# Kernel tuning notes

Measured on AMD Instinct MI355X. Metric: run time of the kernel, lower is better.

The kernel has to match this reference:

```python
import jax, jax.numpy as jnp
import numpy as np

N_NODES = 50000
N_EDGES = 800000
IN_F, HID, OUT_F = 128, 128, 64


def setup_inputs() -> dict:
    key = jax.random.key(0)
    k1, k2, k3, k4 = jax.random.split(key, 4)
    x = jax.random.normal(k1, (N_NODES, IN_F), dtype=jnp.float32)
    edge_index = jax.random.randint(k2, (2, N_EDGES), 0, N_NODES, dtype=jnp.int64)
    # Glorot-style scaled weights, zero bias (PyG GCNConv default)
    W1 = jax.random.normal(k3, (IN_F, HID), dtype=jnp.float32) * (1.0 / np.sqrt(IN_F))
    b1 = jnp.zeros((HID,), dtype=jnp.float32)
    W2 = jax.random.normal(k4, (HID, OUT_F), dtype=jnp.float32) * (1.0 / np.sqrt(HID))
    b2 = jnp.zeros((OUT_F,), dtype=jnp.float32)
    return {"x": x, "edge_index": edge_index, "W1": W1, "b1": b1, "W2": W2, "b2": b2}


def reference(x, edge_index, W1, b1, W2, b2):
    n = x.shape[0]
    # add self-loops (PyG GCNConv default add_self_loops=True)
    loop = jnp.arange(n, dtype=edge_index.dtype)
    src = jnp.concatenate([edge_index[0], loop])  # message source nodes
    dst = jnp.concatenate([edge_index[1], loop])  # aggregation target nodes
    # symmetric normalization: D^{-1/2} (A+I) D^{-1/2}
    deg = jax.ops.segment_sum(jnp.ones(dst.shape, dtype=x.dtype), dst, num_segments=n)
    dinv = jnp.where(deg > 0, jax.lax.rsqrt(deg), 0.0)
    norm = dinv[src] * dinv[dst]  # [E+N]

    def gcn_conv(h, W, b):
        h = h @ W                              # dense transform first (PyG order)
        msg = h[src] * norm[:, None]           # gather + scale: [E+N, d]
        agg = jax.ops.segment_sum(msg, dst, num_segments=n)  # scatter-add
        return agg + b

    h = jax.nn.relu(gcn_conv(x, W1, b1))
    return gcn_conv(h, W2, b2)
```

## Files before the change

### kernel.cpp

```cpp
#include <hip/hip_runtime.h>
#include <hip/hip_bf16.h>

#define NN   50000
#define NE   800000
#define F_IN 128
#define F_H  128
#define F_O  64

#define BINSHIFT 7
#define NBINS    ((NN + 127) >> 7)
#define CAP      2816
#define EPB      2048
#define RPSTRIDE 132

static constexpr int NB_G1  = (NN + 63) / 64;
static constexpr int NB_BIN = (NE + EPB - 1) / EPB;

typedef __bf16 bf16_8 __attribute__((ext_vector_type(8)));
typedef float  f32x4  __attribute__((ext_vector_type(4)));

template <typename AT, int K, int NOUT>
__device__ __forceinline__ void gemm_body(const AT* __restrict__ X,
                                          const float* __restrict__ W,
                                          __hip_bfloat16* __restrict__ Y,
                                          __hip_bfloat16* WB, int blk) {
    constexpr int NKS = K / 32;
    constexpr int NC  = NOUT / 16;
    const int t = threadIdx.x;
    for (int f = t; f < K * NOUT; f += 256) {
        int k = f / NOUT, n = f % NOUT;
        int ks = k >> 5, kr = k & 31, qq = kr >> 3, jj = kr & 7;
        int c = n >> 4, nn = n & 15;
        WB[(((ks * NC + c) * 16 + nn) * 4 + qq) * 8 + jj] = __float2bfloat16(W[f]);
    }
    __syncthreads();

    const int wave = t >> 6, lane = t & 63;
    const int r = lane & 15, q = lane >> 4;
    const int m0 = blk * 64 + wave * 16;
    int arow = m0 + r;
    if (arow >= NN) arow = NN - 1;

    f32x4 acc[NC];
#pragma unroll
    for (int c = 0; c < NC; ++c) acc[c] = (f32x4){0.f, 0.f, 0.f, 0.f};

#pragma unroll
    for (int ks = 0; ks < NKS; ++ks) {
        bf16_8 a;
        if constexpr (sizeof(AT) == 4) {
            const float* xp = (const float*)X + (size_t)arow * K + ks * 32 + q * 8;
            float4 x0 = ((const float4*)xp)[0];
            float4 x1 = ((const float4*)xp)[1];
            a[0] = (__bf16)x0.x; a[1] = (__bf16)x0.y; a[2] = (__bf16)x0.z; a[3] = (__bf16)x0.w;
            a[4] = (__bf16)x1.x; a[5] = (__bf16)x1.y; a[6] = (__bf16)x1.z; a[7] = (__bf16)x1.w;
        } else {
            a = *(const bf16_8*)((const __hip_bfloat16*)X + (size_t)arow * K + ks * 32 + q * 8);
        }
#pragma unroll
        for (int c = 0; c < NC; ++c) {
            bf16_8 b = *(const bf16_8*)&WB[(((ks * NC + c) * 16 + r) * 4 + q) * 8];
            acc[c] = __builtin_amdgcn_mfma_f32_16x16x32_bf16(a, b, acc[c], 0, 0, 0);
        }
    }

#pragma unroll
    for (int c = 0; c < NC; ++c) {
#pragma unroll
        for (int i = 0; i < 4; ++i) {
            int gr = m0 + q * 4 + i;
            if (gr < NN)
                Y[(size_t)gr * NOUT + c * 16 + r] = __float2bfloat16(acc[c][i]);
        }
    }
}

__global__ __launch_bounds__(256) void k_fuseA(const float* __restrict__ X,
                                               const float* __restrict__ W1,
                                               __hip_bfloat16* __restrict__ Xw,
                                               const int* __restrict__ ei32,
                                               int* __restrict__ binbuf,
                                               unsigned* __restrict__ bincnt,
                                               unsigned* __restrict__ cnt) {
    __shared__ __align__(16) char smem[32768];
    const int t = threadIdx.x;

    if (blockIdx.x >= NB_BIN) {
        gemm_body<float, F_IN, F_H>(X, W1, Xw, (__hip_bfloat16*)smem,
                                    blockIdx.x - NB_BIN);
        return;
    }

    unsigned* hist = (unsigned*)smem;
    unsigned* base = hist + NBINS;
    unsigned* rank = base + NBINS;
    for (int i = t; i < NBINS; i += 256) { hist[i] = 0u; rank[i] = 0u; }
    __syncthreads();

    const bool is64 = ((ei32[1] | ei32[3] | ei32[5] | ei32[7]) == 0);
    const int e0 = blockIdx.x * EPB;
    int pk[8], bin[8], dd[8];
#pragma unroll
    for (int j = 0; j < 8; ++j) {
        int e = e0 + t + j * 256;
        if (e < NE) {
            int s, d;
            if (is64) {
                const long long* p = (const long long*)ei32;
                s = (int)p[e];
                d = (int)p[NE + e];
            } else {
                s = ei32[e];
                d = ei32[NE + e];
            }
            pk[j]  = (s << BINSHIFT) | (d & 127);
            bin[j] = d >> BINSHIFT;
            dd[j]  = d;
        } else bin[j] = -1;
    }
#pragma unroll
    for (int j = 0; j < 8; ++j) {
        if (bin[j] >= 0) {
            atomicAdd(&hist[bin[j]], 1u);
            atomicAdd(&cnt[dd[j]], 1u);
        }
    }
    __syncthreads();
    for (int b = t; b < NBINS; b += 256)
        base[b] = atomicAdd(&bincnt[b], hist[b]);
    __syncthreads();
#pragma unroll
    for (int j = 0; j < 8; ++j) {
        if (bin[j] >= 0) {
            unsigned rk = atomicAdd(&rank[bin[j]], 1u);
            binbuf[(size_t)bin[j] * CAP + base[bin[j]] + rk] = pk[j];
        }
    }
}

#define HS 136
__global__ __launch_bounds__(1024) void k_phaseC(const int* __restrict__ binbuf,
                                                 const unsigned* __restrict__ bincnt,
                                                 const unsigned* __restrict__ cnt,
                                                 const __hip_bfloat16* __restrict__ Xw,
                                                 const float* __restrict__ W2,
                                                 const float* __restrict__ b1,
                                                 __hip_bfloat16* __restrict__ Hw,
                                                 int* __restrict__ srcs_g,
                                                 unsigned short* __restrict__ rp_g) {
    __shared__ __align__(16) char smem[64000];
    __hip_bfloat16* Htile = (__hip_bfloat16*)smem;
    __hip_bfloat16* WB2   = (__hip_bfloat16*)(smem + 34816);
    int*      srcsL = (int*)(smem + 34816 + 16384);
    unsigned* h     = (unsigned*)(smem + 62464);
    unsigned* cur   = (unsigned*)(smem + 62976);
    float*    dv    = (float*)(smem + 63488);

    const int b = blockIdx.x, t = threadIdx.x;

    for (int f = t; f < F_H * F_O; f += 1024) {
        int k = f / F_O, n = f % F_O;
        int ks = k >> 5, kr = k & 31, qq = kr >> 3, jj = kr & 7;
        int c = n >> 4, nn = n & 15;
        WB2[(((ks * 4 + c) * 16 + nn) * 4 + qq) * 8 + jj] = __float2bfloat16(W2[f]);
    }
    if (t < 128) h[t] = 0u;
    __syncthreads();

    const unsigned n = bincnt[b];
    const int* buf = binbuf + (size_t)b * CAP;
    for (unsigned i = t; i < n; i += 1024)
        atomicAdd(&h[buf[i] & 127], 1u);
    __syncthreads();
    if (t < 128) cur[t] = h[t];
    __syncthreads();
    for (int off = 1; off < 128; off <<= 1) {
        unsigned u = (t < 128 && t >= off) ? cur[t - off] : 0u;
        __syncthreads();
        if (t < 128) cur[t] += u;
        __syncthreads();
    }
    if (t < 128) {
        unsigned ex = cur[t] - h[t];
        rp_g[b * RPSTRIDE + t] = (unsigned short)ex;
        if (t == 0) rp_g[b * RPSTRIDE + 128] = (unsigned short)n;
        dv[t]  = rsqrtf((float)(h[t] + 1u));
        cur[t] = ex;
    }
    __syncthreads();
    for (unsigned i = t; i < n; i += 1024) {
        int p = buf[i];
        unsigned pos = atomicAdd(&cur[p & 127], 1u);
        int s = p >> BINSHIFT;
        srcsL[pos] = s;
        srcs_g[(size_t)b * CAP + pos] = s;
    }
    __syncthreads();

    const int wave = t >> 6, lane = t & 63;
    const int fl = lane & 15, sub = lane >> 4;
    const float4 b1a = ((const float4*)b1)[fl * 2];
    const float4 b1b = ((const float4*)b1)[fl * 2 + 1];
    for (int nd = 0; nd < 8; ++nd) {
        const int tl    = wave * 8 + nd;
        const int gnode = (b << BINSHIFT) + tl;
        const unsigned i1 = cur[tl];
        const unsigned i0 = i1 - h[tl];
        float acc0[8], acc1[8];
        {
            int sv = (gnode < NN) ? gnode : 0;
            bf16_8 r = *(const bf16_8*)(Xw + (size_t)sv * F_H + fl * 8);
            float w = (sub == 0 && gnode < NN) ? dv[tl] : 0.f;
#pragma unroll
            for (int j = 0; j < 8; ++j) { acc0[j] = w * (float)r[j]; acc1[j] = 0.f; }
        }
        unsigned i = i0 + sub;
        for (; i + 4 < i1; i += 8) {
            int s0 = srcsL[i], s1 = srcsL[i + 4];
            float w0 = rsqrtf((float)(cnt[s0] + 1u));
            float w1 = rsqrtf((float)(cnt[s1] + 1u));
            bf16_8 r0 = *(const bf16_8*)(Xw + (size_t)s0 * F_H + fl * 8);
            bf16_8 r1 = *(const bf16_8*)(Xw + (size_t)s1 * F_H + fl * 8);
#pragma unroll
            for (int j = 0; j < 8; ++j) {
                acc0[j] += w0 * (float)r0[j];
                acc1[j] += w1 * (float)r1[j];
            }
        }
        if (i < i1) {
            int s = srcsL[i];
            float w = rsqrtf((float)(cnt[s] + 1u));
            bf16_8 r = *(const bf16_8*)(Xw + (size_t)s * F_H + fl * 8);
#pragma unroll
            for (int j = 0; j < 8; ++j) acc0[j] += w * (float)r[j];
        }
#pragma unroll
        for (int j = 0; j < 8; ++j) {
            float a = acc0[j] + acc1[j];
            a += __shfl_xor(a, 16, 64);
            a += __shfl_xor(a, 32, 64);
            acc0[j] = a;
        }
        if (sub == 0) {
            const float bias[8] = {b1a.x, b1a.y, b1a.z, b1a.w, b1b.x, b1b.y, b1b.z, b1b.w};
            bf16_8 o;
#pragma unroll
            for (int j = 0; j < 8; ++j)
                o[j] = (__bf16)fmaxf(dv[tl] * acc0[j] + bias[j], 0.f);
            *(bf16_8*)(Htile + tl * HS + fl * 8) = o;
        }
    }
    __syncthreads();

    {
        const int r = lane & 15, q = lane >> 4;
        const int rt = wave >> 1;
        const int c0 = (wave & 1) * 2;
        f32x4 acc[2] = {(f32x4){0.f, 0.f, 0.f, 0.f}, (f32x4){0.f, 0.f, 0.f, 0.f}};
#pragma unroll
        for (int ks = 0; ks < 4; ++ks) {
            bf16_8 a = *(const bf16_8*)(Htile + (rt * 16 + r) * HS + ks * 32 + q * 8);
#pragma unroll
            for (int cc = 0; cc < 2; ++cc) {
                bf16_8 bb = *(const bf16_8*)&WB2[(((ks * 4 + (c0 + cc)) * 16 + r) * 4 + q) * 8];
                acc[cc] = __builtin_amdgcn_mfma_f32_16x16x32_bf16(a, bb, acc[cc], 0, 0, 0);
            }
        }
#pragma unroll
        for (int cc = 0; cc < 2; ++cc) {
#pragma unroll
            for (int i = 0; i < 4; ++i) {
                int tl = rt * 16 + q * 4 + i;
                int gnode = (b << BINSHIFT) + tl;
                if (gnode < NN)
                    Hw[(size_t)gnode * F_O + (c0 + cc) * 16 + r] =
                        __float2bfloat16(dv[tl] * acc[cc][i]);
            }
        }
    }
}

__global__ __launch_bounds__(256) void k_agg2(const __hip_bfloat16* __restrict__ Hw,
                                              const int* __restrict__ srcs_g,
                                              const unsigned short* __restrict__ rp_g,
                                              const float* __restrict__ b2,
                                              float* __restrict__ out) {
    const int wv   = (blockIdx.x * 256 + threadIdx.x) >> 6;
    const int lane = threadIdx.x & 63;
    if (wv >= NN) return;
    const int bin = wv >> BINSHIFT, tl = wv & 127;
    const int sub = lane >> 3;
    const int fl  = lane & 7;
    const unsigned i0 = rp_g[bin * RPSTRIDE + tl];
    const unsigned i1 = rp_g[bin * RPSTRIDE + tl + 1];
    const int* srcs = srcs_g + (size_t)bin * CAP;

    float acc0[8], acc1[8];
    bf16_8 self = *(const bf16_8*)(Hw + (size_t)wv * F_O + fl * 8);
#pragma unroll
    for (int j = 0; j < 8; ++j) {
        acc0[j] = (sub == 0) ? (float)self[j] : 0.f;
        acc1[j] = 0.f;
    }

    unsigned i = i0 + sub;
    for (; i + 8 < i1; i += 16) {
        int s0 = srcs[i], s1 = srcs[i + 8];
        bf16_8 r0 = *(const bf16_8*)(Hw + (size_t)s0 * F_O + fl * 8);
        bf16_8 r1 = *(const bf16_8*)(Hw + (size_t)s1 * F_O + fl * 8);
#pragma unroll
        for (int j = 0; j < 8; ++j) {
            acc0[j] += (float)r0[j];
            acc1[j] += (float)r1[j];
        }
    }
    if (i < i1) {
        int s = srcs[i];
        bf16_8 r = *(const bf16_8*)(Hw + (size_t)s * F_O + fl * 8);
#pragma unroll
        for (int j = 0; j < 8; ++j) acc0[j] += (float)r[j];
    }
#pragma unroll
    for (int j = 0; j < 8; ++j) {
        float a = acc0[j] + acc1[j];
        a += __shfl_xor(a, 8, 64);
        a += __shfl_xor(a, 16, 64);
        a += __shfl_xor(a, 32, 64);
        acc0[j] = a;
    }
    if (sub == 0) {
        float dn = rsqrtf((float)(i1 - i0 + 1u));
        float4 o0 = make_float4(dn * acc0[0] + b2[fl * 8 + 0], dn * acc0[1] + b2[fl * 8 + 1],
                                dn * acc0[2] + b2[fl * 8 + 2], dn * acc0[3] + b2[fl * 8 + 3]);
        float4 o1 = make_float4(dn * acc0[4] + b2[fl * 8 + 4], dn * acc0[5] + b2[fl * 8 + 5],
                                dn * acc0[6] + b2[fl * 8 + 6], dn * acc0[7] + b2[fl * 8 + 7]);
        float4* op = (float4*)(out + (size_t)wv * F_O + fl * 8);
        op[0] = o0;
        op[1] = o1;
    }
}

extern "C" void kernel_launch(void* const* d_in, const int* in_sizes, int n_in,
                              void* d_out, int out_size, void* d_ws, size_t ws_size,
                              hipStream_t stream) {
    const float* x  = (const float*)d_in[0];
    const int*   ei = (const int*)d_in[1];
    const float* W1 = (const float*)d_in[2];
    const float* b1 = (const float*)d_in[3];
    const float* W2 = (const float*)d_in[4];
    const float* b2 = (const float*)d_in[5];
    float* out = (float*)d_out;

    char* w = (char*)d_ws;
    size_t off = 0;
    auto alloc = [&](size_t bytes) {
        void* p = w + off;
        off += (bytes + 255) & ~(size_t)255;
        return p;
    };
    unsigned* cnt     = (unsigned*)alloc((size_t)NN * 4);
    unsigned* bincnt  = (unsigned*)alloc((size_t)NBINS * 4);
    int*      binbuf  = (int*)alloc((size_t)NBINS * CAP * 4);
    int*      srcs    = (int*)alloc((size_t)NBINS * CAP * 4);
    unsigned short* rp = (unsigned short*)alloc((size_t)NBINS * RPSTRIDE * 2);
    __hip_bfloat16* Xw = (__hip_bfloat16*)alloc((size_t)NN * F_H * 2);
    __hip_bfloat16* Hw = (__hip_bfloat16*)alloc((size_t)NN * F_O * 2);

    size_t zlen = (((size_t)NN * 4 + 255) & ~(size_t)255) + (size_t)NBINS * 4;
    hipMemsetAsync(cnt, 0, zlen, stream);

    k_fuseA<<<NB_BIN + NB_G1, 256, 0, stream>>>(x, W1, Xw, ei, binbuf, bincnt, cnt);
    k_phaseC<<<NBINS, 1024, 0, stream>>>(binbuf, bincnt, cnt, Xw, W2, b1, Hw, srcs, rp);
    k_agg2<<<(NN + 3) / 4, 256, 0, stream>>>(Hw, srcs, rp, b2, out);
}
```

Baseline: 199.4 us.

## Fuse phase C and layer-2 aggregation into cooperative kernel with grid syncs

Replaces the global atomic bin counters and the memset with per-block local binning, where each block writes its own prefix-sum table and segment. The second and third kernels are merged into one cooperative kernel with 391 blocks of 512 threads. It gathers each bin's edges from all block segments, builds a CSR in LDS, publishes dinv globally, and uses grid.sync between layer 1, the W2 GEMM and layer 2, so the CSR stays in shared memory. This removes the memset, one launch and the global srcs/rp round trip. In exchange it adds a binary-search gather, two grid-wide barriers and a requirement that all 391 blocks are co-resident.

```diff
diff --git a/kernel.cpp b/kernel.cpp
--- a/kernel.cpp
+++ b/kernel.cpp
@@ -1,5 +1,8 @@
 #include <hip/hip_runtime.h>
 #include <hip/hip_bf16.h>
+#include <hip/hip_cooperative_groups.h>
+
+namespace cg = cooperative_groups;
 
 #define NN   50000
 #define NE   800000
@@ -10,34 +13,35 @@
 #define BINSHIFT 7
 #define NBINS    ((NN + 127) >> 7)
 #define CAP      2816
-#define EPB      2048
-#define RPSTRIDE 132
-
-static constexpr int NB_G1  = (NN + 63) / 64;
-static constexpr int NB_BIN = (NE + EPB - 1) / EPB;
+#define EPB      8192
+#define RSS      (NBINS + 1)
+#define HS       132
+
+static constexpr int NB_GEMM = (NN + 127) / 128;
+static constexpr int NB_BIN  = (NE + EPB - 1) / EPB;
 
 typedef __bf16 bf16_8 __attribute__((ext_vector_type(8)));
 typedef float  f32x4  __attribute__((ext_vector_type(4)));
 
 template <typename AT, int K, int NOUT>
-__device__ __forceinline__ void gemm_body(const AT* __restrict__ X,
-                                          const float* __restrict__ W,
-                                          __hip_bfloat16* __restrict__ Y,
-                                          __hip_bfloat16* WB, int blk) {
+__device__ __forceinline__ void gemm_body512(const AT* __restrict__ X,
+                                             const float* __restrict__ W,
+                                             __hip_bfloat16* __restrict__ Y,
+                                             __hip_bfloat16* WB, int blk) {
     constexpr int NKS = K / 32;
     constexpr int NC  = NOUT / 16;
     const int t = threadIdx.x;
-    for (int f = t; f < K * NOUT; f += 256) {
+    for (int f = t; f < K * NOUT; f += 512) {
         int k = f / NOUT, n = f % NOUT;
         int ks = k >> 5, kr = k & 31, qq = kr >> 3, jj = kr & 7;
         int c = n >> 4, nn = n & 15;
-        WB[(((ks * NC + c) * 16 + nn) * 4 + qq) * 8 + jj] = __float2bfloat16(W[f]);
+        WB[(((ks * NC + c) * 4 + qq) * 16 + nn) * 8 + jj] = __float2bfloat16(W[f]);
     }
     __syncthreads();
 
     const int wave = t >> 6, lane = t & 63;
     const int r = lane & 15, q = lane >> 4;
-    const int m0 = blk * 64 + wave * 16;
+    const int m0 = blk * 128 + wave * 16;
     int arow = m0 + r;
     if (arow >= NN) arow = NN - 1;
 
@@ -59,7 +63,7 @@
         }
 #pragma unroll
         for (int c = 0; c < NC; ++c) {
-            bf16_8 b = *(const bf16_8*)&WB[(((ks * NC + c) * 16 + r) * 4 + q) * 8];
+            bf16_8 b = *(const bf16_8*)&WB[(((ks * NC + c) * 4 + q) * 16 + r) * 8];
             acc[c] = __builtin_amdgcn_mfma_f32_16x16x32_bf16(a, b, acc[c], 0, 0, 0);
         }
     }
@@ -75,102 +79,122 @@
     }
 }
 
-__global__ __launch_bounds__(256) void k_fuseA(const float* __restrict__ X,
+__global__ __launch_bounds__(512) void k_fuseA(const float* __restrict__ X,
                                                const float* __restrict__ W1,
                                                __hip_bfloat16* __restrict__ Xw,
                                                const int* __restrict__ ei32,
                                                int* __restrict__ binbuf,
-                                               unsigned* __restrict__ bincnt,
-                                               unsigned* __restrict__ cnt) {
+                                               unsigned* __restrict__ rs) {
     __shared__ __align__(16) char smem[32768];
     const int t = threadIdx.x;
 
     if (blockIdx.x >= NB_BIN) {
-        gemm_body<float, F_IN, F_H>(X, W1, Xw, (__hip_bfloat16*)smem,
-                                    blockIdx.x - NB_BIN);
+        gemm_body512<float, F_IN, F_H>(X, W1, Xw, (__hip_bfloat16*)smem,
+                                       blockIdx.x - NB_BIN);
         return;
     }
 
     unsigned* hist = (unsigned*)smem;
-    unsigned* base = hist + NBINS;
-    unsigned* rank = base + NBINS;
-    for (int i = t; i < NBINS; i += 256) { hist[i] = 0u; rank[i] = 0u; }
+    unsigned* ofs  = hist + 512;
+    for (int i = t; i < NBINS; i += 512) hist[i] = 0u;
     __syncthreads();
 
     const bool is64 = ((ei32[1] | ei32[3] | ei32[5] | ei32[7]) == 0);
+    const long long* p64 = (const long long*)ei32;
     const int e0 = blockIdx.x * EPB;
-    int pk[8], bin[8], dd[8];
-#pragma unroll
-    for (int j = 0; j < 8; ++j) {
-        int e = e0 + t + j * 256;
-        if (e < NE) {
-            int s, d;
-            if (is64) {
-                const long long* p = (const long long*)ei32;
-                s = (int)p[e];
-                d = (int)p[NE + e];
-            } else {
-                s = ei32[e];
-                d = ei32[NE + e];
-            }
-            pk[j]  = (s << BINSHIFT) | (d & 127);
-            bin[j] = d >> BINSHIFT;
-            dd[j]  = d;
-        } else bin[j] = -1;
-    }
-#pragma unroll
-    for (int j = 0; j < 8; ++j) {
-        if (bin[j] >= 0) {
-            atomicAdd(&hist[bin[j]], 1u);
-            atomicAdd(&cnt[dd[j]], 1u);
-        }
-    }
-    __syncthreads();
-    for (int b = t; b < NBINS; b += 256)
-        base[b] = atomicAdd(&bincnt[b], hist[b]);
-    __syncthreads();
-#pragma unroll
-    for (int j = 0; j < 8; ++j) {
-        if (bin[j] >= 0) {
-            unsigned rk = atomicAdd(&rank[bin[j]], 1u);
-            binbuf[(size_t)bin[j] * CAP + base[bin[j]] + rk] = pk[j];
-        }
+    const int e1 = (e0 + EPB < NE) ? e0 + EPB : NE;
+
+    for (int e = e0 + t; e < e1; e += 512) {
+        int d = is64 ? (int)p64[NE + e] : ei32[NE + e];
+        atomicAdd(&hist[d >> BINSHIFT], 1u);
+    }
+    __syncthreads();
+
+    unsigned v = (t < NBINS) ? hist[t] : 0u;
+    ofs[t] = v;
+    __syncthreads();
+    for (int off = 1; off < 512; off <<= 1) {
+        unsigned u = (t >= off) ? ofs[t - off] : 0u;
+        __syncthreads();
+        ofs[t] += u;
+        __syncthreads();
+    }
+    if (t < NBINS) {
+        unsigned ex = ofs[t] - v;
+        rs[blockIdx.x * RSS + t] = ex;
+        hist[t] = ex;
+    }
+    if (t == 0) rs[blockIdx.x * RSS + NBINS] = (unsigned)(e1 - e0);
+    __syncthreads();
+
+    for (int e = e0 + t; e < e1; e += 512) {
+        int s, d;
+        if (is64) { s = (int)p64[e]; d = (int)p64[NE + e]; }
+        else      { s = ei32[e];     d = ei32[NE + e]; }
+        unsigned pos = atomicAdd(&hist[d >> BINSHIFT], 1u);
+        binbuf[e0 + pos] = (s << BINSHIFT) | (d & 127);
     }
 }
 
-#define HS 136
-__global__ __launch_bounds__(1024) void k_phaseC(const int* __restrict__ binbuf,
-                                                 const unsigned* __restrict__ bincnt,
-                                                 const unsigned* __restrict__ cnt,
-                                                 const __hip_bfloat16* __restrict__ Xw,
-                                                 const float* __restrict__ W2,
-                                                 const float* __restrict__ b1,
-                                                 __hip_bfloat16* __restrict__ Hw,
-                                                 int* __restrict__ srcs_g,
-                                                 unsigned short* __restrict__ rp_g) {
-    __shared__ __align__(16) char smem[64000];
+__global__ __launch_bounds__(512) void k_mega(const int* __restrict__ binbuf,
+                                              const unsigned* __restrict__ rs,
+                                              const __hip_bfloat16* __restrict__ Xw,
+                                              const float* __restrict__ W2,
+                                              const float* __restrict__ b1,
+                                              const float* __restrict__ b2,
+                                              float* __restrict__ dinvG,
+                                              __hip_bfloat16* __restrict__ Hw,
+                                              float* __restrict__ out) {
+    cg::grid_group grid = cg::this_grid();
+
+    __shared__ __align__(16) char smem[64512];
     __hip_bfloat16* Htile = (__hip_bfloat16*)smem;
-    __hip_bfloat16* WB2   = (__hip_bfloat16*)(smem + 34816);
-    int*      srcsL = (int*)(smem + 34816 + 16384);
-    unsigned* h     = (unsigned*)(smem + 62464);
-    unsigned* cur   = (unsigned*)(smem + 62976);
-    float*    dv    = (float*)(smem + 63488);
-
-    const int b = blockIdx.x, t = threadIdx.x;
-
-    for (int f = t; f < F_H * F_O; f += 1024) {
-        int k = f / F_O, n = f % F_O;
-        int ks = k >> 5, kr = k & 31, qq = kr >> 3, jj = kr & 7;
-        int c = n >> 4, nn = n & 15;
-        WB2[(((ks * 4 + c) * 16 + nn) * 4 + qq) * 8 + jj] = __float2bfloat16(W2[f]);
-    }
-    if (t < 128) h[t] = 0u;
-    __syncthreads();
-
-    const unsigned n = bincnt[b];
-    const int* buf = binbuf + (size_t)b * CAP;
-    for (unsigned i = t; i < n; i += 1024)
-        atomicAdd(&h[buf[i] & 127], 1u);
+    int*      srcsL = (int*)smem;
+    int*      csrL  = (int*)(smem + 33792);
+    __hip_bfloat16* W2B = (__hip_bfloat16*)(smem + 45056);
+    unsigned* stL  = (unsigned*)(smem + 61440);
+    unsigned* lenL = (unsigned*)(smem + 61952);
+    unsigned* lofs = (unsigned*)(smem + 62464);
+    unsigned* h    = (unsigned*)(smem + 62976);
+    unsigned* cur  = (unsigned*)(smem + 63488);
+    float*    dv   = (float*)(smem + 64000);
+
+    const int bb = blockIdx.x, t = threadIdx.x;
+    const int wave = t >> 6, lane = t & 63;
+
+    if (t < 128) {
+        unsigned s0 = 0, ln = 0;
+        if (t < NB_BIN) {
+            s0 = rs[t * RSS + bb];
+            ln = rs[t * RSS + bb + 1] - s0;
+        }
+        stL[t] = s0;
+        lenL[t] = ln;
+        lofs[t] = ln;
+        h[t] = 0u;
+    }
+    __syncthreads();
+    for (int off = 1; off < 128; off <<= 1) {
+        unsigned u = (t < 128 && t >= off) ? lofs[t - off] : 0u;
+        __syncthreads();
+        if (t < 128) lofs[t] += u;
+        __syncthreads();
+    }
+    const unsigned n = lofs[NB_BIN - 1];
+
+    for (unsigned i = t; i < n; i += 512) {
+        int lo = 0, hi = NB_BIN - 1;
+        while (lo < hi) {
+            int mid = (lo + hi) >> 1;
+            if (lofs[mid] > i) hi = mid; else lo = mid + 1;
+        }
+        unsigned within = i - (lofs[lo] - lenL[lo]);
+        srcsL[i] = binbuf[lo * EPB + stL[lo] + within];
+    }
+    __syncthreads();
+
+    for (unsigned i = t; i < n; i += 512)
+        atomicAdd(&h[srcsL[i] & 127], 1u);
     __syncthreads();
     if (t < 128) cur[t] = h[t];
     __syncthreads();
@@ -182,161 +206,177 @@
     }
     if (t < 128) {
         unsigned ex = cur[t] - h[t];
-        rp_g[b * RPSTRIDE + t] = (unsigned short)ex;
-        if (t == 0) rp_g[b * RPSTRIDE + 128] = (unsigned short)n;
-        dv[t]  = rsqrtf((float)(h[t] + 1u));
+        int node = (bb << BINSHIFT) + t;
+        float d = rsqrtf((float)(h[t] + 1u));
+        dv[t] = d;
+        if (node < NN) dinvG[node] = d;
         cur[t] = ex;
     }
     __syncthreads();
-    for (unsigned i = t; i < n; i += 1024) {
-        int p = buf[i];
+    for (unsigned i = t; i < n; i += 512) {
+        int p = srcsL[i];
         unsigned pos = atomicAdd(&cur[p & 127], 1u);
-        int s = p >> BINSHIFT;
-        srcsL[pos] = s;
-        srcs_g[(size_t)b * CAP + pos] = s;
-    }
-    __syncthreads();
-
-    const int wave = t >> 6, lane = t & 63;
-    const int fl = lane & 15, sub = lane >> 4;
-    const float4 b1a = ((const float4*)b1)[fl * 2];
-    const float4 b1b = ((const float4*)b1)[fl * 2 + 1];
-    for (int nd = 0; nd < 8; ++nd) {
-        const int tl    = wave * 8 + nd;
-        const int gnode = (b << BINSHIFT) + tl;
-        const unsigned i1 = cur[tl];
-        const unsigned i0 = i1 - h[tl];
-        float acc0[8], acc1[8];
+        csrL[pos] = p >> BINSHIFT;
+    }
+
+    grid.sync();
+
+    {
+        const int sub = lane >> 4, fl = lane & 15;
+        float b1r[8];
         {
-            int sv = (gnode < NN) ? gnode : 0;
-            bf16_8 r = *(const bf16_8*)(Xw + (size_t)sv * F_H + fl * 8);
-            float w = (sub == 0 && gnode < NN) ? dv[tl] : 0.f;
-#pragma unroll
-            for (int j = 0; j < 8; ++j) { acc0[j] = w * (float)r[j]; acc1[j] = 0.f; }
-        }
-        unsigned i = i0 + sub;
-        for (; i + 4 < i1; i += 8) {
-            int s0 = srcsL[i], s1 = srcsL[i + 4];
-            float w0 = rsqrtf((float)(cnt[s0] + 1u));
-            float w1 = rsqrtf((float)(cnt[s1] + 1u));
-            bf16_8 r0 = *(const bf16_8*)(Xw + (size_t)s0 * F_H + fl * 8);
-            bf16_8 r1 = *(const bf16_8*)(Xw + (size_t)s1 * F_H + fl * 8);
+            float4 ba = ((const float4*)b1)[fl * 2];
+            float4 bbv = ((const float4*)b1)[fl * 2 + 1];
+            b1r[0] = ba.x; b1r[1] = ba.y; b1r[2] = ba.z; b1r[3] = ba.w;
+            b1r[4] = bbv.x; b1r[5] = bbv.y; b1r[6] = bbv.z; b1r[7] = bbv.w;
+        }
+        for (int k = 0; k < 16; ++k) {
+            const int tl = k * 8 + wave;
+            const int gnode = (bb << BINSHIFT) + tl;
+            const unsigned i1 = cur[tl];
+            const unsigned i0 = i1 - h[tl];
+            const float dn = dv[tl];
+            int srow = (gnode < NN) ? gnode : 0;
+            bf16_8 self = *(const bf16_8*)(Xw + (size_t)srow * F_H + fl * 8);
+            float acc0[8], acc1[8];
 #pragma unroll
             for (int j = 0; j < 8; ++j) {
-                acc0[j] += w0 * (float)r0[j];
-                acc1[j] += w1 * (float)r1[j];
-            }
-        }
-        if (i < i1) {
-            int s = srcsL[i];
-            float w = rsqrtf((float)(cnt[s] + 1u));
-            bf16_8 r = *(const bf16_8*)(Xw + (size_t)s * F_H + fl * 8);
-#pragma unroll
-            for (int j = 0; j < 8; ++j) acc0[j] += w * (float)r[j];
-        }
-#pragma unroll
-        for (int j = 0; j < 8; ++j) {
-            float a = acc0[j] + acc1[j];
-            a += __shfl_xor(a, 16, 64);
-            a += __shfl_xor(a, 32, 64);
-            acc0[j] = a;
-        }
-        if (sub == 0) {
-            const float bias[8] = {b1a.x, b1a.y, b1a.z, b1a.w, b1b.x, b1b.y, b1b.z, b1b.w};
-            bf16_8 o;
-#pragma unroll
-            for (int j = 0; j < 8; ++j)
-                o[j] = (__bf16)fmaxf(dv[tl] * acc0[j] + bias[j], 0.f);
-            *(bf16_8*)(Htile + tl * HS + fl * 8) = o;
-        }
+                acc0[j] = (sub == 0 && gnode < NN) ? dn * (float)self[j] : 0.f;
+                acc1[j] = 0.f;
+            }
+            unsigned i = i0 + sub;
+            for (; i + 4 < i1; i += 8) {
+                int s0 = csrL[i], s1 = csrL[i + 4];
+                float d0 = dinvG[s0], d1 = dinvG[s1];
+                bf16_8 r0 = *(const bf16_8*)(Xw + (size_t)s0 * F_H + fl * 8);
+                bf16_8 r1 = *(const bf16_8*)(Xw + (size_t)s1 * F_H + fl * 8);
+#pragma unroll
+                for (int j = 0; j < 8; ++j) {
+                    acc0[j] += d0 * (float)r0[j];
+                    acc1[j] += d1 * (float)r1[j];
+                }
+            }
+            if (i < i1) {
+                int s = csrL[i];
+                float d = dinvG[s];
+                bf16_8 r = *(const bf16_8*)(Xw + (size_t)s * F_H + fl * 8);
+#pragma unroll
+                for (int j = 0; j < 8; ++j) acc0[j] += d * (float)r[j];
+            }
+#pragma unroll
+            for (int j = 0; j < 8; ++j) {
+                float a = acc0[j] + acc1[j];
+                a += __shfl_xor(a, 16, 64);
+                a += __shfl_xor(a, 32, 64);
+                acc0[j] = a;
+            }
+            if (sub == 0) {
+                bf16_8 o;
+#pragma unroll
+                for (int j = 0; j < 8; ++j) {
+                    float vv = fmaxf(dn * acc0[j] + b1r[j], 0.f);
+                    o[j] = (gnode < NN) ? (__bf16)vv : (__bf16)0.f;
+                }
+                *(bf16_8*)(Htile + tl * HS + fl * 8) = o;
+            }
+        }
+    }
+
+    for (int f = t; f < F_H * F_O; f += 512) {
+        int k = f >> 6, nc = f & 63;
+        int ks = k >> 5, kr = k & 31, qq = kr >> 3, jj = kr & 7;
+        int c = nc >> 4, nn = nc & 15;
+        W2B[(((ks * 4 + c) * 4 + qq) * 16 + nn) * 8 + jj] = __float2bfloat16(W2[f]);
     }
     __syncthreads();
 
     {
         const int r = lane & 15, q = lane >> 4;
-        const int rt = wave >> 1;
-        const int c0 = (wave & 1) * 2;
-        f32x4 acc[2] = {(f32x4){0.f, 0.f, 0.f, 0.f}, (f32x4){0.f, 0.f, 0.f, 0.f}};
+        const int rt = wave;
+        f32x4 acc[4];
+#pragma unroll
+        for (int c = 0; c < 4; ++c) acc[c] = (f32x4){0.f, 0.f, 0.f, 0.f};
 #pragma unroll
         for (int ks = 0; ks < 4; ++ks) {
             bf16_8 a = *(const bf16_8*)(Htile + (rt * 16 + r) * HS + ks * 32 + q * 8);
 #pragma unroll
-            for (int cc = 0; cc < 2; ++cc) {
-                bf16_8 bb = *(const bf16_8*)&WB2[(((ks * 4 + (c0 + cc)) * 16 + r) * 4 + q) * 8];
-                acc[cc] = __builtin_amdgcn_mfma_f32_16x16x32_bf16(a, bb, acc[cc], 0, 0, 0);
-            }
-        }
-#pragma unroll
-        for (int cc = 0; cc < 2; ++cc) {
+            for (int c = 0; c < 4; ++c) {
+                bf16_8 bfr = *(const bf16_8*)&W2B[(((ks * 4 + c) * 4 + q) * 16 + r) * 8];
+                acc[c] = __builtin_amdgcn_mfma_f32_16x16x32_bf16(a, bfr, acc[c], 0, 0, 0);
+            }
+        }
+#pragma unroll
+        for (int c = 0; c < 4; ++c) {
 #pragma unroll
             for (int i = 0; i < 4; ++i) {
                 int tl = rt * 16 + q * 4 + i;
-                int gnode = (b << BINSHIFT) + tl;
+                int gnode = (bb << BINSHIFT) + tl;
                 if (gnode < NN)
-                    Hw[(size_t)gnode * F_O + (c0 + cc) * 16 + r] =
-                        __float2bfloat16(dv[tl] * acc[cc][i]);
-            }
-        }
-    }
-}
-
-__global__ __launch_bounds__(256) void k_agg2(const __hip_bfloat16* __restrict__ Hw,
-                                              const int* __restrict__ srcs_g,
-                                              const unsigned short* __restrict__ rp_g,
-                                              const float* __restrict__ b2,
-                                              float* __restrict__ out) {
-    const int wv   = (blockIdx.x * 256 + threadIdx.x) >> 6;
-    const int lane = threadIdx.x & 63;
-    if (wv >= NN) return;
-    const int bin = wv >> BINSHIFT, tl = wv & 127;
-    const int sub = lane >> 3;
-    const int fl  = lane & 7;
-    const unsigned i0 = rp_g[bin * RPSTRIDE + tl];
-    const unsigned i1 = rp_g[bin * RPSTRIDE + tl + 1];
-    const int* srcs = srcs_g + (size_t)bin * CAP;
-
-    float acc0[8], acc1[8];
-    bf16_8 self = *(const bf16_8*)(Hw + (size_t)wv * F_O + fl * 8);
-#pragma unroll
-    for (int j = 0; j < 8; ++j) {
-        acc0[j] = (sub == 0) ? (float)self[j] : 0.f;
-        acc1[j] = 0.f;
-    }
-
-    unsigned i = i0 + sub;
-    for (; i + 8 < i1; i += 16) {
-        int s0 = srcs[i], s1 = srcs[i + 8];
-        bf16_8 r0 = *(const bf16_8*)(Hw + (size_t)s0 * F_O + fl * 8);
-        bf16_8 r1 = *(const bf16_8*)(Hw + (size_t)s1 * F_O + fl * 8);
-#pragma unroll
-        for (int j = 0; j < 8; ++j) {
-            acc0[j] += (float)r0[j];
-            acc1[j] += (float)r1[j];
-        }
-    }
-    if (i < i1) {
-        int s = srcs[i];
-        bf16_8 r = *(const bf16_8*)(Hw + (size_t)s * F_O + fl * 8);
-#pragma unroll
-        for (int j = 0; j < 8; ++j) acc0[j] += (float)r[j];
-    }
-#pragma unroll
-    for (int j = 0; j < 8; ++j) {
-        float a = acc0[j] + acc1[j];
-        a += __shfl_xor(a, 8, 64);
-        a += __shfl_xor(a, 16, 64);
-        a += __shfl_xor(a, 32, 64);
-        acc0[j] = a;
-    }
-    if (sub == 0) {
-        float dn = rsqrtf((float)(i1 - i0 + 1u));
-        float4 o0 = make_float4(dn * acc0[0] + b2[fl * 8 + 0], dn * acc0[1] + b2[fl * 8 + 1],
-                                dn * acc0[2] + b2[fl * 8 + 2], dn * acc0[3] + b2[fl * 8 + 3]);
-        float4 o1 = make_float4(dn * acc0[4] + b2[fl * 8 + 4], dn * acc0[5] + b2[fl * 8 + 5],
-                                dn * acc0[6] + b2[fl * 8 + 6], dn * acc0[7] + b2[fl * 8 + 7]);
-        float4* op = (float4*)(out + (size_t)wv * F_O + fl * 8);
-        op[0] = o0;
-        op[1] = o1;
+                    Hw[(size_t)gnode * F_O + c * 16 + r] =
+                        __float2bfloat16(dv[tl] * acc[c][i]);
+            }
+        }
+    }
+
+    grid.sync();
+
+    {
+        const int sub = lane >> 3, fl = lane & 7;
+        float b2r[8];
+        {
+            float4 ba = ((const float4*)b2)[fl * 2];
+            float4 bbv = ((const float4*)b2)[fl * 2 + 1];
+            b2r[0] = ba.x; b2r[1] = ba.y; b2r[2] = ba.z; b2r[3] = ba.w;
+            b2r[4] = bbv.x; b2r[5] = bbv.y; b2r[6] = bbv.z; b2r[7] = bbv.w;
+        }
+        for (int k = 0; k < 16; ++k) {
+            const int tl = k * 8 + wave;
+            const int gnode = (bb << BINSHIFT) + tl;
+            if (gnode >= NN) continue;
+            const unsigned i1 = cur[tl];
+            const unsigned i0 = i1 - h[tl];
+            bf16_8 self = *(const bf16_8*)(Hw + (size_t)gnode * F_O + fl * 8);
+            float acc0[8], acc1[8];
+#pragma unroll
+            for (int j = 0; j < 8; ++j) {
+                acc0[j] = (sub == 0) ? (float)self[j] : 0.f;
+                acc1[j] = 0.f;
+            }
+            unsigned i = i0 + sub;
+            for (; i + 8 < i1; i += 16) {
+                int s0 = csrL[i], s1 = csrL[i + 8];
+                bf16_8 r0 = *(const bf16_8*)(Hw + (size_t)s0 * F_O + fl * 8);
+                bf16_8 r1 = *(const bf16_8*)(Hw + (size_t)s1 * F_O + fl * 8);
+#pragma unroll
+                for (int j = 0; j < 8; ++j) {
+                    acc0[j] += (float)r0[j];
+                    acc1[j] += (float)r1[j];
+                }
+            }
+            if (i < i1) {
+                bf16_8 r = *(const bf16_8*)(Hw + (size_t)csrL[i] * F_O + fl * 8);
+#pragma unroll
+                for (int j = 0; j < 8; ++j) acc0[j] += (float)r[j];
+            }
+#pragma unroll
+            for (int j = 0; j < 8; ++j) {
+                float a = acc0[j] + acc1[j];
+                a += __shfl_xor(a, 8, 64);
+                a += __shfl_xor(a, 16, 64);
+                a += __shfl_xor(a, 32, 64);
+                acc0[j] = a;
+            }
+            if (sub == 0) {
+                float dn = dv[tl];
+                float4 o0 = make_float4(dn * acc0[0] + b2r[0], dn * acc0[1] + b2r[1],
+                                        dn * acc0[2] + b2r[2], dn * acc0[3] + b2r[3]);
+                float4 o1 = make_float4(dn * acc0[4] + b2r[4], dn * acc0[5] + b2r[5],
+                                        dn * acc0[6] + b2r[6], dn * acc0[7] + b2r[7]);
+                float4* op = (float4*)(out + (size_t)gnode * F_O + fl * 8);
+                op[0] = o0;
+                op[1] = o1;
+            }
+        }
     }
 }
 
@@ -358,18 +398,15 @@
         off += (bytes + 255) & ~(size_t)255;
         return p;
     };
-    unsigned* cnt     = (unsigned*)alloc((size_t)NN * 4);
-    unsigned* bincnt  = (unsigned*)alloc((size_t)NBINS * 4);
-    int*      binbuf  = (int*)alloc((size_t)NBINS * CAP * 4);
-    int*      srcs    = (int*)alloc((size_t)NBINS * CAP * 4);
-    unsigned short* rp = (unsigned short*)alloc((size_t)NBINS * RPSTRIDE * 2);
+    int*      binbuf = (int*)alloc((size_t)NB_BIN * EPB * 4);
+    unsigned* rs     = (unsigned*)alloc((size_t)NB_BIN * RSS * 4);
+    float*    dinv   = (float*)alloc((size_t)NN * 4);
     __hip_bfloat16* Xw = (__hip_bfloat16*)alloc((size_t)NN * F_H * 2);
     __hip_bfloat16* Hw = (__hip_bfloat16*)alloc((size_t)NN * F_O * 2);
 
-    size_t zlen = (((size_t)NN * 4 + 255) & ~(size_t)255) + (size_t)NBINS * 4;
-    hipMemsetAsync(cnt, 0, zlen, stream);
-
-    k_fuseA<<<NB_BIN + NB_G1, 256, 0, stream>>>(x, W1, Xw, ei, binbuf, bincnt, cnt);
-    k_phaseC<<<NBINS, 1024, 0, stream>>>(binbuf, bincnt, cnt, Xw, W2, b1, Hw, srcs, rp);
-    k_agg2<<<(NN + 3) / 4, 256, 0, stream>>>(Hw, srcs, rp, b2, out);
+    k_fuseA<<<NB_BIN + NB_GEMM, 512, 0, stream>>>(x, W1, Xw, ei, binbuf, rs);
+
+    void* kargs[] = {(void*)&binbuf, (void*)&rs, (void*)&Xw, (void*)&W2,
+                     (void*)&b1, (void*)&b2, (void*)&dinv, (void*)&Hw, (void*)&out};
+    hipLaunchCooperativeKernel((void*)k_mega, dim3(NBINS), dim3(512), kargs, 0, stream);
 }
```

After: 270.5 us. 1.36x slower.
